# Kernel optimization log

Measured on AMD Instinct MI355X. Metric: run time of the kernel, lower is better.

## Reference

```python
import jax, jax.numpy as jnp
import numpy as np

HIDDEN = 768
NUM_LABELS = 64


def setup_inputs() -> dict:
    key = jax.random.key(0)
    k1, k2, k3, k4, k5 = jax.random.split(key, 5)
    B, S = 16, 4096
    com_features = jax.random.normal(k1, (B, S, HIDDEN), dtype=jnp.float32)
    labels = jax.random.randint(k2, (B, S), 0, NUM_LABELS + 1, dtype=jnp.int64)
    label_feature = jax.random.normal(k3, (NUM_LABELS, HIDDEN), dtype=jnp.float32)
    # nn.Linear(1536, 768): weight [out, in], bias [out]
    merge_w = jax.random.normal(k4, (HIDDEN, 2 * HIDDEN), dtype=jnp.float32) * (1.0 / np.sqrt(2 * HIDDEN))
    merge_b = jax.random.normal(k5, (HIDDEN,), dtype=jnp.float32) * 0.01
    return {"com_features": com_features, "labels": labels,
            "label_feature": label_feature, "merge_w": merge_w, "merge_b": merge_b}


def reference(com_features, labels, label_feature, merge_w, merge_b):
    B, S, H = com_features.shape
    tokens_emb = com_features.reshape(-1, H)          # [N, H]
    token_labels = labels.reshape(-1)                  # [N]
    active = token_labels != 0                         # label 0 = inactive
    # label_id = label - 1 indexes the concatenated label-feature table.
    # Clip so inactive rows gather a valid (ignored) row; result is masked out.
    label_id = jnp.clip(token_labels - 1, 0, label_feature.shape[0] - 1)
    centers = label_feature[label_id]                  # [N, H] gather
    # merge(cat(token_emb, center)) == token @ W_left^T + center @ W_right^T + b
    cat = jnp.concatenate([tokens_emb, centers], axis=-1)  # [N, 2H]
    merged = cat @ merge_w.T + merge_b                 # [N, H]
    # scatter_ back into token embeddings: active rows replaced by merged.
    out = jnp.where(active[:, None], merged, tokens_emb)
    return out.reshape(B, S, H)
```

## Files before the change

### kernel.cpp

```cpp
#include <hip/hip_runtime.h>
#include <hip/hip_bf16.h>

#define HID 768
#define WROW 1536
#define NLAB 64

typedef __attribute__((ext_vector_type(8))) __bf16 bf16x8;
typedef __attribute__((ext_vector_type(4))) float f32x4;

__device__ __forceinline__ bf16x8 pk8(float4 a, float4 b) {
    return (bf16x8){(__bf16)a.x, (__bf16)a.y, (__bf16)a.z, (__bf16)a.w,
                    (__bf16)b.x, (__bf16)b.y, (__bf16)b.z, (__bf16)b.w};
}

__device__ __forceinline__ void async16(const void* g, void* l) {
    __builtin_amdgcn_global_load_lds(
        (const __attribute__((address_space(1))) void*)g,
        (__attribute__((address_space(3))) void*)l,
        16, 0, 0);
}

__global__ __launch_bounds__(256) void cvtA_kernel(
    const float* __restrict__ src, unsigned short* __restrict__ dst, long n8)
{
    long i = (long)blockIdx.x * 256 + threadIdx.x;
    const long stride = (long)gridDim.x * 256;
    for (; i < n8; i += stride) {
        float4 a = *(const float4*)(src + i * 8);
        float4 b = *(const float4*)(src + i * 8 + 4);
        *(bf16x8*)(dst + i * 8) = pk8(a, b);
    }
}

__global__ __launch_bounds__(256) void cvtW_kernel(
    const float* __restrict__ W, unsigned short* __restrict__ Wb)
{
    const int u = blockIdx.x * 256 + threadIdx.x;
    const int j = u / 96;
    const int c = (u % 96) * 8;
    float4 a = *(const float4*)(W + (size_t)j * WROW + c);
    float4 b = *(const float4*)(W + (size_t)j * WROW + c + 4);
    *(bf16x8*)(Wb + (size_t)j * HID + c) = pk8(a, b);
}

__global__ __launch_bounds__(256) void compute_P_kernel(
    const float* __restrict__ lf,
    const float* __restrict__ W,
    const float* __restrict__ bias,
    float* __restrict__ P)
{
    const int j = blockIdx.x;
    const int t = threadIdx.x;
    __shared__ __align__(16) float wrow[HID];
    if (t < 192)
        *(float4*)(wrow + t * 4) =
            *(const float4*)(W + (size_t)j * WROW + HID + t * 4);
    __syncthreads();

    const int lab = t >> 2;
    const int seg = t & 3;
    const float* lfp = lf + lab * HID + seg * 192;
    const float* wp  = wrow + seg * 192;
    float acc = 0.f;
    #pragma unroll 8
    for (int i = 0; i < 192; i += 4) {
        float4 u = *(const float4*)(lfp + i);
        float4 v = *(const float4*)(wp + i);
        acc += u.x * v.x + u.y * v.y + u.z * v.z + u.w * v.w;
    }
    acc += __shfl_xor(acc, 1);
    acc += __shfl_xor(acc, 2);
    if (seg == 0) P[lab * HID + j] = acc + bias[j];
}

__global__ __launch_bounds__(256) void merge_gemm_bf16_kernel(
    const unsigned short* __restrict__ Ab,
    const float* __restrict__ A,
    const int* __restrict__ labels,
    const unsigned short* __restrict__ Wb,
    const float* __restrict__ P,
    float* __restrict__ out,
    const int nwg)
{
    __shared__ __align__(16) unsigned short As[2][128 * 32];
    __shared__ __align__(16) unsigned short Bs[2][128 * 32];
    __shared__ int Ls[128];

    int bid = blockIdx.x;
    {
        const int q = nwg >> 3;
        bid = (bid & 7) * q + (bid >> 3);
    }
    const int m0 = (bid / (HID / 128)) * 128;
    const int j0 = (bid % (HID / 128)) * 128;

    const int t = threadIdx.x;
    if (t < 128) Ls[t] = labels[m0 + t];

    const int w  = t >> 6;
    const int l  = t & 63;
    const int lm = l & 15;
    const int lk = l >> 4;
    const int qm = (w >> 1) * 64;
    const int qn = (w & 1) * 64;

    const unsigned short* gA = Ab + (size_t)(m0 + (t >> 2)) * HID + (t & 3) * 8;
    const unsigned short* gB = Wb + (size_t)(j0 + (t >> 2)) * HID + (t & 3) * 8;

    f32x4 acc[4][4] = {};

#define STAGE(buf, K) do { \
    async16(gA + (K),                    &As[buf][t * 8]);        \
    async16(gA + (size_t)64 * HID + (K), &As[buf][t * 8 + 2048]); \
    async16(gB + (K),                    &Bs[buf][t * 8]);        \
    async16(gB + (size_t)64 * HID + (K), &Bs[buf][t * 8 + 2048]); \
} while (0)

#define COMPUTE(buf) do { \
    bf16x8 af[4], bfr[4]; \
    _Pragma("unroll") \
    for (int mi = 0; mi < 4; ++mi) \
        af[mi] = *(const bf16x8*)&As[buf][(qm + mi * 16 + lm) * 32 + lk * 8]; \
    _Pragma("unroll") \
    for (int ni = 0; ni < 4; ++ni) \
        bfr[ni] = *(const bf16x8*)&Bs[buf][(qn + ni * 16 + lm) * 32 + lk * 8]; \
    _Pragma("unroll") \
    for (int mi = 0; mi < 4; ++mi) \
        _Pragma("unroll") \
        for (int ni = 0; ni < 4; ++ni) \
            acc[mi][ni] = __builtin_amdgcn_mfma_f32_16x16x32_bf16( \
                af[mi], bfr[ni], acc[mi][ni], 0, 0, 0); \
} while (0)

    STAGE(0, 0);
    int cur = 0;
    __syncthreads();
    for (int k0 = 32; k0 < HID; k0 += 32) {
        STAGE(cur ^ 1, k0);
        COMPUTE(cur);
        __syncthreads();
        cur ^= 1;
    }
    COMPUTE(cur);
#undef STAGE
#undef COMPUTE

    #pragma unroll
    for (int mi = 0; mi < 4; ++mi) {
        const int rowb = qm + mi * 16 + lk * 4;
        #pragma unroll
        for (int r = 0; r < 4; ++r) {
            const int n_tok = m0 + rowb + r;
            const int lab   = Ls[rowb + r];
            const size_t rowoff = (size_t)n_tok * HID;
            #pragma unroll
            for (int ni = 0; ni < 4; ++ni) {
                const int j = j0 + qn + ni * 16 + lm;
                float v;
                if (lab != 0)
                    v = acc[mi][ni][r] + P[(size_t)(lab - 1) * HID + j];
                else
                    v = A[rowoff + j];
                out[rowoff + j] = v;
            }
        }
    }
}

__global__ __launch_bounds__(256) void merge_gemm_kernel(
    const float* __restrict__ A,
    const int* __restrict__ labels,
    const float* __restrict__ W,
    const float* __restrict__ P,
    float* __restrict__ out,
    const int nwg)
{
    __shared__ __align__(16) unsigned short As[2][128 * 32];
    __shared__ __align__(16) unsigned short Bs[2][128 * 32];
    __shared__ int Ls[128];

    int bid = blockIdx.x;
    if ((nwg & 7) == 0) {
        const int q = nwg >> 3;
        bid = (bid & 7) * q + (bid >> 3);
    }
    const int m0 = (bid / (HID / 128)) * 128;
    const int j0 = (bid % (HID / 128)) * 128;

    const int t = threadIdx.x;
    if (t < 128) Ls[t] = labels[m0 + t];

    const int w  = t >> 6;
    const int l  = t & 63;
    const int lm = l & 15;
    const int lk = l >> 4;
    const int qm = (w >> 1) * 64;
    const int qn = (w & 1) * 64;

    const int sr = t >> 2;
    const int sc = t & 3;
    const float* gA  = A + (size_t)(m0 + sr) * HID  + sc * 8;
    const float* gA2 = gA + (size_t)64 * HID;
    const float* gB  = W + (size_t)(j0 + sr) * WROW + sc * 8;
    const float* gB2 = gB + (size_t)64 * WROW;
    const int eoff = sr * 32 + ((sc ^ (sr & 3)) * 8);

    float4 ra0, ra1, ra2, ra3, rb0, rb1, rb2, rb3;
    f32x4 acc[4][4] = {};

#define ISSUE(K) do { \
    ra0 = *(const float4*)(gA  + (K));      ra1 = *(const float4*)(gA  + (K) + 4); \
    ra2 = *(const float4*)(gA2 + (K));      ra3 = *(const float4*)(gA2 + (K) + 4); \
    rb0 = *(const float4*)(gB  + (K));      rb1 = *(const float4*)(gB  + (K) + 4); \
    rb2 = *(const float4*)(gB2 + (K));      rb3 = *(const float4*)(gB2 + (K) + 4); \
} while (0)

    ISSUE(0);
    int p = 0;
    for (int k0 = 0; k0 < HID; k0 += 32) {
        *(bf16x8*)&As[p][eoff]        = pk8(ra0, ra1);
        *(bf16x8*)&As[p][eoff + 2048] = pk8(ra2, ra3);
        *(bf16x8*)&Bs[p][eoff]        = pk8(rb0, rb1);
        *(bf16x8*)&Bs[p][eoff + 2048] = pk8(rb2, rb3);
        if (k0 + 32 < HID) ISSUE(k0 + 32);
        __syncthreads();

        bf16x8 af[4], bfr[4];
        #pragma unroll
        for (int mi = 0; mi < 4; ++mi) {
            const int r = qm + mi * 16 + lm;
            af[mi] = *(const bf16x8*)&As[p][r * 32 + ((lk ^ (r & 3)) * 8)];
        }
        #pragma unroll
        for (int ni = 0; ni < 4; ++ni) {
            const int r = qn + ni * 16 + lm;
            bfr[ni] = *(const bf16x8*)&Bs[p][r * 32 + ((lk ^ (r & 3)) * 8)];
        }
        #pragma unroll
        for (int mi = 0; mi < 4; ++mi)
            #pragma unroll
            for (int ni = 0; ni < 4; ++ni)
                acc[mi][ni] = __builtin_amdgcn_mfma_f32_16x16x32_bf16(
                    af[mi], bfr[ni], acc[mi][ni], 0, 0, 0);
        p ^= 1;
    }
#undef ISSUE

    #pragma unroll
    for (int mi = 0; mi < 4; ++mi) {
        const int rowb = qm + mi * 16 + lk * 4;
        #pragma unroll
        for (int r = 0; r < 4; ++r) {
            const int n_tok = m0 + rowb + r;
            const int lab   = Ls[rowb + r];
            const size_t rowoff = (size_t)n_tok * HID;
            #pragma unroll
            for (int ni = 0; ni < 4; ++ni) {
                const int j = j0 + qn + ni * 16 + lm;
                float v;
                if (lab != 0)
                    v = acc[mi][ni][r] + P[(size_t)(lab - 1) * HID + j];
                else
                    v = A[rowoff + j];
                out[rowoff + j] = v;
            }
        }
    }
}

extern "C" void kernel_launch(void* const* d_in, const int* in_sizes, int n_in,
                              void* d_out, int out_size, void* d_ws, size_t ws_size,
                              hipStream_t stream) {
    const float* com    = (const float*)d_in[0];
    const int*   labels = (const int*)d_in[1];
    const float* lf     = (const float*)d_in[2];
    const float* W      = (const float*)d_in[3];
    const float* bias   = (const float*)d_in[4];
    float* out = (float*)d_out;

    const int n_rows = in_sizes[0] / HID;
    const int nwg = (n_rows / 128) * (HID / 128);

    float* P = (float*)d_ws;
    const size_t off_Wb = (size_t)NLAB * HID * 4;
    const size_t off_Ab = off_Wb + (size_t)HID * HID * 2;
    const size_t need   = off_Ab + (size_t)n_rows * HID * 2;

    if (ws_size >= need) {
        unsigned short* Wb = (unsigned short*)((char*)d_ws + off_Wb);
        unsigned short* Ab = (unsigned short*)((char*)d_ws + off_Ab);
        const long n8 = (long)n_rows * HID / 8;
        cvtA_kernel<<<dim3(2048), dim3(256), 0, stream>>>(com, Ab, n8);
        cvtW_kernel<<<dim3(HID * 96 / 256), dim3(256), 0, stream>>>(W, Wb);
        compute_P_kernel<<<dim3(HID), dim3(256), 0, stream>>>(lf, W, bias, P);
        merge_gemm_bf16_kernel<<<dim3(nwg), dim3(256), 0, stream>>>(
            Ab, com, labels, Wb, P, out, nwg);
    } else {
        compute_P_kernel<<<dim3(HID), dim3(256), 0, stream>>>(lf, W, bias, P);
        merge_gemm_kernel<<<dim3(nwg), dim3(256), 0, stream>>>(
            com, labels, W, P, out, nwg);
    }
}
```

Measured before the change: 531.2 us.

## Use 256x256 tiles with 512 threads and triple-buffered async LDS pipeline

Replaces the 128x128 bf16 GEMM with a 256x256 tile kernel using 8 waves, a three-stage global_load_lds ring with explicit vmcnt waits, an XOR swizzle on LDS k-chunks, and raised MFMA priority. The larger tile is meant to raise arithmetic intensity and cut redundant reads of A and W. The deeper pipeline is meant to hide memory latency. In exchange it uses more LDS and registers per block and launches far fewer blocks (768), which may hurt occupancy and tail balance.

```diff
diff --git a/kernel.cpp b/kernel.cpp
--- a/kernel.cpp
+++ b/kernel.cpp
@@ -4,6 +4,7 @@
 #define HID 768
 #define WROW 1536
 #define NLAB 64
+#define NT   24
 
 typedef __attribute__((ext_vector_type(8))) __bf16 bf16x8;
 typedef __attribute__((ext_vector_type(4))) float f32x4;
@@ -44,10 +45,8 @@
 }
 
 __global__ __launch_bounds__(256) void compute_P_kernel(
-    const float* __restrict__ lf,
-    const float* __restrict__ W,
-    const float* __restrict__ bias,
-    float* __restrict__ P)
+    const float* __restrict__ lf, const float* __restrict__ W,
+    const float* __restrict__ bias, float* __restrict__ P)
 {
     const int j = blockIdx.x;
     const int t = threadIdx.x;
@@ -73,7 +72,7 @@
     if (seg == 0) P[lab * HID + j] = acc + bias[j];
 }
 
-__global__ __launch_bounds__(256) void merge_gemm_bf16_kernel(
+__global__ __launch_bounds__(512, 2) void merge_gemm_v2_kernel(
     const unsigned short* __restrict__ Ab,
     const float* __restrict__ A,
     const int* __restrict__ labels,
@@ -82,12 +81,110 @@
     float* __restrict__ out,
     const int nwg)
 {
+    __shared__ __align__(16) unsigned short As[3][256 * 32];
+    __shared__ __align__(16) unsigned short Bs[3][256 * 32];
+    __shared__ int Ls[256];
+
+    int bid = blockIdx.x;
+    {
+        const int q = nwg >> 3;
+        bid = (bid & 7) * q + (bid >> 3);
+    }
+    const int m0 = (bid / 3) * 256;
+    const int j0 = (bid % 3) * 256;
+
+    const int t = threadIdx.x;
+    if (t < 256) Ls[t] = labels[m0 + t];
+
+    const int wid = t >> 6;
+    const int l   = t & 63;
+    const int lm  = l & 15;
+    const int lk  = l >> 4;
+    const int wm  = wid >> 2;
+    const int wn  = wid & 3;
+
+    const int srow = t >> 2;
+    const int scol = ((t & 3) ^ ((t >> 3) & 3)) * 8;
+    const unsigned short* gA = Ab + (size_t)(m0 + srow) * HID + scol;
+    const unsigned short* gB = Wb + (size_t)(j0 + srow) * HID + scol;
+
+    const int kchunk = (lk ^ ((lm >> 1) & 3)) * 8;
+
+    f32x4 acc[8][4] = {};
+
+#define STAGE(slot, KT) do {                                                   \
+    const size_t kc = (size_t)(KT) * 32;                                       \
+    async16(gA + kc,                      &As[slot][t * 8]);                   \
+    async16(gA + (size_t)128 * HID + kc,  &As[slot][4096 + t * 8]);            \
+    async16(gB + kc,                      &Bs[slot][t * 8]);                   \
+    async16(gB + (size_t)128 * HID + kc,  &Bs[slot][4096 + t * 8]);            \
+} while (0)
+
+    STAGE(0, 0);
+    STAGE(1, 1);
+    __syncthreads();
+
+    for (int kt = 0; kt < NT; ++kt) {
+        const int b = kt % 3;
+        if (kt + 2 < NT) STAGE((kt + 2) % 3, kt + 2);
+
+        bf16x8 af[8], bf[4];
+        #pragma unroll
+        for (int mi = 0; mi < 8; ++mi)
+            af[mi] = *(const bf16x8*)&As[b][(wm * 128 + mi * 16 + lm) * 32 + kchunk];
+        #pragma unroll
+        for (int ni = 0; ni < 4; ++ni)
+            bf[ni] = *(const bf16x8*)&Bs[b][(wn * 64 + ni * 16 + lm) * 32 + kchunk];
+
+        __builtin_amdgcn_s_setprio(1);
+        #pragma unroll
+        for (int mi = 0; mi < 8; ++mi)
+            #pragma unroll
+            for (int ni = 0; ni < 4; ++ni)
+                acc[mi][ni] = __builtin_amdgcn_mfma_f32_16x16x32_bf16(
+                    af[mi], bf[ni], acc[mi][ni], 0, 0, 0);
+        __builtin_amdgcn_s_setprio(0);
+
+        if (kt + 2 < NT)
+            asm volatile("s_waitcnt vmcnt(4)\n\ts_barrier" ::: "memory");
+        else
+            asm volatile("s_waitcnt vmcnt(0)\n\ts_barrier" ::: "memory");
+    }
+#undef STAGE
+
+    #pragma unroll
+    for (int mi = 0; mi < 8; ++mi) {
+        const int rowb = wm * 128 + mi * 16 + lk * 4;
+        #pragma unroll
+        for (int r = 0; r < 4; ++r) {
+            const int row   = rowb + r;
+            const int lab   = Ls[row];
+            const size_t rowoff = (size_t)(m0 + row) * HID;
+            #pragma unroll
+            for (int ni = 0; ni < 4; ++ni) {
+                const int j = j0 + wn * 64 + ni * 16 + lm;
+                float v;
+                if (lab != 0)
+                    v = acc[mi][ni][r] + P[(size_t)(lab - 1) * HID + j];
+                else
+                    v = A[rowoff + j];
+                out[rowoff + j] = v;
+            }
+        }
+    }
+}
+
+__global__ __launch_bounds__(256) void merge_gemm_kernel(
+    const float* __restrict__ A, const int* __restrict__ labels,
+    const float* __restrict__ W, const float* __restrict__ P,
+    float* __restrict__ out, const int nwg)
+{
     __shared__ __align__(16) unsigned short As[2][128 * 32];
     __shared__ __align__(16) unsigned short Bs[2][128 * 32];
     __shared__ int Ls[128];
 
     int bid = blockIdx.x;
-    {
+    if ((nwg & 7) == 0) {
         const int q = nwg >> 3;
         bid = (bid & 7) * q + (bid >> 3);
     }
@@ -104,55 +201,62 @@
     const int qm = (w >> 1) * 64;
     const int qn = (w & 1) * 64;
 
-    const unsigned short* gA = Ab + (size_t)(m0 + (t >> 2)) * HID + (t & 3) * 8;
-    const unsigned short* gB = Wb + (size_t)(j0 + (t >> 2)) * HID + (t & 3) * 8;
-
+    const int sr = t >> 2;
+    const int sc = t & 3;
+    const float* gA  = A + (size_t)(m0 + sr) * HID  + sc * 8;
+    const float* gA2 = gA + (size_t)64 * HID;
+    const float* gB  = W + (size_t)(j0 + sr) * WROW + sc * 8;
+    const float* gB2 = gB + (size_t)64 * WROW;
+    const int eoff = sr * 32 + ((sc ^ (sr & 3)) * 8);
+
+    float4 ra0, ra1, ra2, ra3, rb0, rb1, rb2, rb3;
     f32x4 acc[4][4] = {};
 
-#define STAGE(buf, K) do { \
-    async16(gA + (K),                    &As[buf][t * 8]);        \
-    async16(gA + (size_t)64 * HID + (K), &As[buf][t * 8 + 2048]); \
-    async16(gB + (K),                    &Bs[buf][t * 8]);        \
-    async16(gB + (size_t)64 * HID + (K), &Bs[buf][t * 8 + 2048]); \
+#define ISSUE(K) do { \
+    ra0 = *(const float4*)(gA  + (K));      ra1 = *(const float4*)(gA  + (K) + 4); \
+    ra2 = *(const float4*)(gA2 + (K));      ra3 = *(const float4*)(gA2 + (K) + 4); \
+    rb0 = *(const float4*)(gB  + (K));      rb1 = *(const float4*)(gB  + (K) + 4); \
+    rb2 = *(const float4*)(gB2 + (K));      rb3 = *(const float4*)(gB2 + (K) + 4); \
 } while (0)
 
-#define COMPUTE(buf) do { \
-    bf16x8 af[4], bfr[4]; \
-    _Pragma("unroll") \
-    for (int mi = 0; mi < 4; ++mi) \
-        af[mi] = *(const bf16x8*)&As[buf][(qm + mi * 16 + lm) * 32 + lk * 8]; \
-    _Pragma("unroll") \
-    for (int ni = 0; ni < 4; ++ni) \
-        bfr[ni] = *(const bf16x8*)&Bs[buf][(qn + ni * 16 + lm) * 32 + lk * 8]; \
-    _Pragma("unroll") \
-    for (int mi = 0; mi < 4; ++mi) \
-        _Pragma("unroll") \
-        for (int ni = 0; ni < 4; ++ni) \
-            acc[mi][ni] = __builtin_amdgcn_mfma_f32_16x16x32_bf16( \
-                af[mi], bfr[ni], acc[mi][ni], 0, 0, 0); \
-} while (0)
-
-    STAGE(0, 0);
-    int cur = 0;
-    __syncthreads();
-    for (int k0 = 32; k0 < HID; k0 += 32) {
-        STAGE(cur ^ 1, k0);
-        COMPUTE(cur);
+    ISSUE(0);
+    int p = 0;
+    for (int k0 = 0; k0 < HID; k0 += 32) {
+        *(bf16x8*)&As[p][eoff]        = pk8(ra0, ra1);
+        *(bf16x8*)&As[p][eoff + 2048] = pk8(ra2, ra3);
+        *(bf16x8*)&Bs[p][eoff]        = pk8(rb0, rb1);
+        *(bf16x8*)&Bs[p][eoff + 2048] = pk8(rb2, rb3);
+        if (k0 + 32 < HID) ISSUE(k0 + 32);
         __syncthreads();
-        cur ^= 1;
-    }
-    COMPUTE(cur);
-#undef STAGE
-#undef COMPUTE
+
+        bf16x8 af[4], bfr[4];
+        #pragma unroll
+        for (int mi = 0; mi < 4; ++mi) {
+            const int r = qm + mi * 16 + lm;
+            af[mi] = *(const bf16x8*)&As[p][r * 32 + ((lk ^ (r & 3)) * 8)];
+        }
+        #pragma unroll
+        for (int ni = 0; ni < 4; ++ni) {
+            const int r = qn + ni * 16 + lm;
+            bfr[ni] = *(const bf16x8*)&Bs[p][r * 32 + ((lk ^ (r & 3)) * 8)];
+        }
+        #pragma unroll
+        for (int mi = 0; mi < 4; ++mi)
+            #pragma unroll
+            for (int ni = 0; ni < 4; ++ni)
+                acc[mi][ni] = __builtin_amdgcn_mfma_f32_16x16x32_bf16(
+                    af[mi], bfr[ni], acc[mi][ni], 0, 0, 0);
+        p ^= 1;
+    }
+#undef ISSUE
 
     #pragma unroll
     for (int mi = 0; mi < 4; ++mi) {
         const int rowb = qm + mi * 16 + lk * 4;
         #pragma unroll
         for (int r = 0; r < 4; ++r) {
-            const int n_tok = m0 + rowb + r;
             const int lab   = Ls[rowb + r];
-            const size_t rowoff = (size_t)n_tok * HID;
+            const size_t rowoff = (size_t)(m0 + rowb + r) * HID;
             #pragma unroll
             for (int ni = 0; ni < 4; ++ni) {
                 const int j = j0 + qn + ni * 16 + lm;
@@ -167,107 +271,6 @@
     }
 }
 
-__global__ __launch_bounds__(256) void merge_gemm_kernel(
-    const float* __restrict__ A,
-    const int* __restrict__ labels,
-    const float* __restrict__ W,
-    const float* __restrict__ P,
-    float* __restrict__ out,
-    const int nwg)
-{
-    __shared__ __align__(16) unsigned short As[2][128 * 32];
-    __shared__ __align__(16) unsigned short Bs[2][128 * 32];
-    __shared__ int Ls[128];
-
-    int bid = blockIdx.x;
-    if ((nwg & 7) == 0) {
-        const int q = nwg >> 3;
-        bid = (bid & 7) * q + (bid >> 3);
-    }
-    const int m0 = (bid / (HID / 128)) * 128;
-    const int j0 = (bid % (HID / 128)) * 128;
-
-    const int t = threadIdx.x;
-    if (t < 128) Ls[t] = labels[m0 + t];
-
-    const int w  = t >> 6;
-    const int l  = t & 63;
-    const int lm = l & 15;
-    const int lk = l >> 4;
-    const int qm = (w >> 1) * 64;
-    const int qn = (w & 1) * 64;
-
-    const int sr = t >> 2;
-    const int sc = t & 3;
-    const float* gA  = A + (size_t)(m0 + sr) * HID  + sc * 8;
-    const float* gA2 = gA + (size_t)64 * HID;
-    const float* gB  = W + (size_t)(j0 + sr) * WROW + sc * 8;
-    const float* gB2 = gB + (size_t)64 * WROW;
-    const int eoff = sr * 32 + ((sc ^ (sr & 3)) * 8);
-
-    float4 ra0, ra1, ra2, ra3, rb0, rb1, rb2, rb3;
-    f32x4 acc[4][4] = {};
-
-#define ISSUE(K) do { \
-    ra0 = *(const float4*)(gA  + (K));      ra1 = *(const float4*)(gA  + (K) + 4); \
-    ra2 = *(const float4*)(gA2 + (K));      ra3 = *(const float4*)(gA2 + (K) + 4); \
-    rb0 = *(const float4*)(gB  + (K));      rb1 = *(const float4*)(gB  + (K) + 4); \
-    rb2 = *(const float4*)(gB2 + (K));      rb3 = *(const float4*)(gB2 + (K) + 4); \
-} while (0)
-
-    ISSUE(0);
-    int p = 0;
-    for (int k0 = 0; k0 < HID; k0 += 32) {
-        *(bf16x8*)&As[p][eoff]        = pk8(ra0, ra1);
-        *(bf16x8*)&As[p][eoff + 2048] = pk8(ra2, ra3);
-        *(bf16x8*)&Bs[p][eoff]        = pk8(rb0, rb1);
-        *(bf16x8*)&Bs[p][eoff + 2048] = pk8(rb2, rb3);
-        if (k0 + 32 < HID) ISSUE(k0 + 32);
-        __syncthreads();
-
-        bf16x8 af[4], bfr[4];
-        #pragma unroll
-        for (int mi = 0; mi < 4; ++mi) {
-            const int r = qm + mi * 16 + lm;
-            af[mi] = *(const bf16x8*)&As[p][r * 32 + ((lk ^ (r & 3)) * 8)];
-        }
-        #pragma unroll
-        for (int ni = 0; ni < 4; ++ni) {
-            const int r = qn + ni * 16 + lm;
-            bfr[ni] = *(const bf16x8*)&Bs[p][r * 32 + ((lk ^ (r & 3)) * 8)];
-        }
-        #pragma unroll
-        for (int mi = 0; mi < 4; ++mi)
-            #pragma unroll
-            for (int ni = 0; ni < 4; ++ni)
-                acc[mi][ni] = __builtin_amdgcn_mfma_f32_16x16x32_bf16(
-                    af[mi], bfr[ni], acc[mi][ni], 0, 0, 0);
-        p ^= 1;
-    }
-#undef ISSUE
-
-    #pragma unroll
-    for (int mi = 0; mi < 4; ++mi) {
-        const int rowb = qm + mi * 16 + lk * 4;
-        #pragma unroll
-        for (int r = 0; r < 4; ++r) {
-            const int n_tok = m0 + rowb + r;
-            const int lab   = Ls[rowb + r];
-            const size_t rowoff = (size_t)n_tok * HID;
-            #pragma unroll
-            for (int ni = 0; ni < 4; ++ni) {
-                const int j = j0 + qn + ni * 16 + lm;
-                float v;
-                if (lab != 0)
-                    v = acc[mi][ni][r] + P[(size_t)(lab - 1) * HID + j];
-                else
-                    v = A[rowoff + j];
-                out[rowoff + j] = v;
-            }
-        }
-    }
-}
-
 extern "C" void kernel_launch(void* const* d_in, const int* in_sizes, int n_in,
                               void* d_out, int out_size, void* d_ws, size_t ws_size,
                               hipStream_t stream) {
@@ -279,7 +282,6 @@
     float* out = (float*)d_out;
 
     const int n_rows = in_sizes[0] / HID;
-    const int nwg = (n_rows / 128) * (HID / 128);
 
     float* P = (float*)d_ws;
     const size_t off_Wb = (size_t)NLAB * HID * 4;
@@ -293,10 +295,12 @@
         cvtA_kernel<<<dim3(2048), dim3(256), 0, stream>>>(com, Ab, n8);
         cvtW_kernel<<<dim3(HID * 96 / 256), dim3(256), 0, stream>>>(W, Wb);
         compute_P_kernel<<<dim3(HID), dim3(256), 0, stream>>>(lf, W, bias, P);
-        merge_gemm_bf16_kernel<<<dim3(nwg), dim3(256), 0, stream>>>(
+        const int nwg = (n_rows / 256) * (HID / 256);
+        merge_gemm_v2_kernel<<<dim3(nwg), dim3(512), 0, stream>>>(
             Ab, com, labels, Wb, P, out, nwg);
     } else {
         compute_P_kernel<<<dim3(HID), dim3(256), 0, stream>>>(lf, W, bias, P);
+        const int nwg = (n_rows / 128) * (HID / 128);
         merge_gemm_kernel<<<dim3(nwg), dim3(256), 0, stream>>>(
             com, labels, W, P, out, nwg);
     }
```

New measurement: 540.1 us. About the same (+1.7%).
